# Performance work log

Measured on AMD Instinct MI355X. Metric: run time of the kernel, lower is better.

## Reference

```python
import jax, jax.numpy as jnp
import numpy as np

H, W = 480, 640
N = 256
CFEAT = 256
FAR = 80.0

def _quat_to_rot(q):
    # q: [N,4] normalized (w,x,y,z)
    w, x, y, z = q[:, 0], q[:, 1], q[:, 2], q[:, 3]
    return jnp.stack([
        jnp.stack([1 - 2 * (y * y + z * z), 2 * (x * y - w * z), 2 * (x * z + w * y)], -1),
        jnp.stack([2 * (x * y + w * z), 1 - 2 * (x * x + z * z), 2 * (y * z - w * x)], -1),
        jnp.stack([2 * (x * z - w * y), 2 * (y * z + w * x), 1 - 2 * (x * x + y * y)], -1)], -2)

def setup_inputs():
    key = jax.random.key(0)
    ks = jax.random.split(key, 10)
    z = jax.random.uniform(ks[0], (N,), minval=2.0, maxval=30.0)
    x = jax.random.uniform(ks[1], (N,), minval=-0.6, maxval=0.6) * z
    y = jax.random.uniform(ks[2], (N,), minval=-0.45, maxval=0.45) * z
    means3d = jnp.stack([x, y, z], -1)                                   # [N,3] in front of camera
    features = jax.random.normal(ks[3], (N, CFEAT))                      # [N,256]
    opacities = jax.random.uniform(ks[4], (N,), minval=0.3, maxval=0.95)
    scales = jax.random.uniform(ks[5], (N, 3), minval=0.05, maxval=0.4)
    rotations = jax.random.normal(ks[6], (N, 4))                         # unnormalized quats
    cam_K = jnp.array([[500.0, 0.0, 320.0], [0.0, 500.0, 240.0], [0.0, 0.0, 1.0]])
    cam_pose = jnp.eye(4)
    w1 = jax.random.normal(ks[7], (CFEAT, 128)) * (1.0 / np.sqrt(CFEAT))
    b1 = jnp.zeros((128,))
    w2 = jax.random.normal(ks[8], (128, 128)) * (1.0 / np.sqrt(128))
    b2 = jnp.zeros((128,))
    w3 = jax.random.normal(ks[9], (128, 12)) * (1.0 / np.sqrt(128))
    b3 = jnp.zeros((12,))
    return dict(means3d=means3d, features=features, opacities=opacities, scales=scales,
                rotations=rotations, cam_K=cam_K, cam_pose=cam_pose,
                w1=w1, b1=b1, w2=w2, b2=b2, w3=w3, b3=b3)

def _render(means3d, features, opacities, scales, rotations, cam_K, cam_pose):
    fx, fy = cam_K[0, 0], cam_K[1, 1]
    cx, cy = cam_K[0, 2], cam_K[1, 2]
    Rw, tw = cam_pose[:3, :3], cam_pose[:3, 3]
    tcam = means3d @ Rw.T + tw                                           # [N,3] camera-frame
    tz = tcam[:, 2]
    valid = tz > 0.01                                                    # near_plane cull
    tzs = jnp.where(valid, tz, 1.0)
    tx, ty = tcam[:, 0], tcam[:, 1]
    # 3D covariance: Sigma = R S S^T R^T
    q = rotations / (jnp.linalg.norm(rotations, axis=1, keepdims=True) + 1e-8)
    Rq = _quat_to_rot(q)                                                 # [N,3,3]
    M = Rq * scales[:, None, :]
    Sigma = jnp.einsum('nij,nkj->nik', M, M)
    Sc = jnp.einsum('ij,njk,lk->nil', Rw, Sigma, Rw)                     # world -> camera
    # EWA projection Jacobian [N,2,3]
    zero = jnp.zeros_like(tzs)
    J = jnp.stack([
        jnp.stack([fx / tzs, zero, -fx * tx / (tzs * tzs)], -1),
        jnp.stack([zero, fy / tzs, -fy * ty / (tzs * tzs)], -1)], -2)
    cov2d = jnp.einsum('nij,njk,nlk->nil', J, Sc, J) + 0.3 * jnp.eye(2)  # low-pass dilation
    a, b, c = cov2d[:, 0, 0], cov2d[:, 0, 1], cov2d[:, 1, 1]
    inv_det = 1.0 / jnp.maximum(a * c - b * b, 1e-12)
    A, B, C = c * inv_det, -b * inv_det, a * inv_det                     # conic
    u = fx * tx / tzs + cx
    v = fy * ty / tzs + cy
    px = jnp.arange(W, dtype=jnp.float32) + 0.5
    py = jnp.arange(H, dtype=jnp.float32) + 0.5
    dx = px[None, :] - u[:, None]                                        # [N,W]
    dy = py[None, :] - v[:, None]                                        # [N,H]
    power = (-(0.5 * A)[:, None, None] * (dx * dx)[:, None, :]
             - (0.5 * C)[:, None, None] * (dy * dy)[:, :, None]
             - B[:, None, None] * dy[:, :, None] * dx[:, None, :])       # [N,H,W]
    alpha = jnp.minimum(0.99, opacities[:, None, None] * jnp.exp(jnp.minimum(power, 0.0)))
    alpha = jnp.where(valid[:, None, None] & (alpha >= 1.0 / 255.0), alpha, 0.0)
    # front-to-back alpha compositing in depth order
    order = jnp.argsort(jnp.where(valid, tz, jnp.inf))
    alpha = jnp.take(alpha, order, axis=0).reshape(N, H * W)
    feats = jnp.take(features, order, axis=0)
    tzo = jnp.take(jnp.where(valid, tz, 0.0), order, axis=0)
    T = jnp.cumprod(1.0 - alpha, axis=0)
    T_excl = jnp.concatenate([jnp.ones((1, H * W), alpha.dtype), T[:-1]], axis=0)
    wgt = T_excl * alpha                                                 # [N,P]
    feat_img = jnp.einsum('np,nc->pc', wgt, feats).reshape(H, W, CFEAT)
    depth_img = jnp.einsum('np,n->p', wgt, tzo).reshape(H, W, 1)
    return feat_img, depth_img

def reference(means3d, features, opacities, scales, rotations, cam_K, cam_pose,
              w1, b1, w2, b2, w3, b3):
    rendered, depth = _render(means3d, features, opacities, scales, rotations, cam_K, cam_pose)
    depth = jnp.clip(depth, 0.0, FAR)
    h = jax.nn.relu(rendered @ w1 + b1)
    h = jax.nn.relu(h @ w2 + b2)
    seg = (h @ w3 + b3)[None]                                            # [1,H,W,12]
    return rendered, depth, seg
```

## Files before the change

### kernel.cpp

```cpp
#include <hip/hip_runtime.h>
#include <stdint.h>

#define HH 480
#define WW 640
#define NG 256
#define CF 256
#define FARV 80.0f
#define TILES_X (WW/64)
#define AST 264
#define BST 136

typedef __attribute__((ext_vector_type(4))) float f32x4;
typedef __attribute__((ext_vector_type(8))) short s16x8;

__device__ __forceinline__ unsigned short f2bf(float f){
  union { float f; unsigned int u; } c; c.f = f;
  unsigned int u = c.u + 0x7fffu + ((c.u >> 16) & 1u);
  return (unsigned short)(u >> 16);
}
__device__ __forceinline__ float bf2f(unsigned short h){
  union { unsigned int u; float f; } c; c.u = ((unsigned int)h) << 16; return c.f;
}

__global__ __launch_bounds__(256) void k_proj(
    const float* __restrict__ means3d,
    const float* __restrict__ opac,
    const float* __restrict__ scales,
    const float* __restrict__ rots,
    const float* __restrict__ camK,
    const float* __restrict__ camP,
    float* __restrict__ wspq,
    int* __restrict__ sidx)
{
  __shared__ float keys[NG];
  const int t = threadIdx.x;

  const float fx = camK[0], fy = camK[4];
  const float cx = camK[2], cy = camK[5];
  float Rw[3][3], tw[3];
#pragma unroll
  for (int r=0;r<3;r++){
#pragma unroll
    for (int c=0;c<3;c++) Rw[r][c] = camP[r*4+c];
    tw[r] = camP[r*4+3];
  }

  float mx = means3d[t*3+0], my = means3d[t*3+1], mz = means3d[t*3+2];
  float tcx = Rw[0][0]*mx + Rw[0][1]*my + Rw[0][2]*mz + tw[0];
  float tcy = Rw[1][0]*mx + Rw[1][1]*my + Rw[1][2]*mz + tw[1];
  float tcz = Rw[2][0]*mx + Rw[2][1]*my + Rw[2][2]*mz + tw[2];
  bool valid = tcz > 0.01f;
  float tzs = valid ? tcz : 1.0f;

  float qw = rots[t*4+0], qx = rots[t*4+1];
  float qy = rots[t*4+2], qz = rots[t*4+3];
  float nrm = sqrtf(qw*qw+qx*qx+qy*qy+qz*qz) + 1e-8f;
  qw /= nrm; qx /= nrm; qy /= nrm; qz /= nrm;
  float Rq[3][3];
  {
    float xx=qx*qx, yy=qy*qy, zz=qz*qz;
    float xy=qx*qy, xz=qx*qz, yz=qy*qz;
    float wx=qw*qx, wy=qw*qy, wz=qw*qz;
    Rq[0][0]=1.f-2.f*(yy+zz); Rq[0][1]=2.f*(xy-wz); Rq[0][2]=2.f*(xz+wy);
    Rq[1][0]=2.f*(xy+wz); Rq[1][1]=1.f-2.f*(xx+zz); Rq[1][2]=2.f*(yz-wx);
    Rq[2][0]=2.f*(xz-wy); Rq[2][1]=2.f*(yz+wx); Rq[2][2]=1.f-2.f*(xx+yy);
  }
  float s0 = scales[t*3+0], s1 = scales[t*3+1], s2 = scales[t*3+2];
  float s0s=s0*s0, s1s=s1*s1, s2s=s2*s2;
  float Sig[3][3];
#pragma unroll
  for (int i=0;i<3;i++)
#pragma unroll
    for (int j=0;j<3;j++)
      Sig[i][j] = s0s*Rq[i][0]*Rq[j][0] + s1s*Rq[i][1]*Rq[j][1] + s2s*Rq[i][2]*Rq[j][2];
  float Tm[3][3];
#pragma unroll
  for (int i=0;i<3;i++)
#pragma unroll
    for (int k=0;k<3;k++)
      Tm[i][k] = Rw[i][0]*Sig[0][k] + Rw[i][1]*Sig[1][k] + Rw[i][2]*Sig[2][k];
  float Sc[3][3];
#pragma unroll
  for (int i=0;i<3;i++)
#pragma unroll
    for (int l=0;l<3;l++)
      Sc[i][l] = Tm[i][0]*Rw[l][0] + Tm[i][1]*Rw[l][1] + Tm[i][2]*Rw[l][2];

  float iz = 1.0f / tzs;
  float r00 = fx*iz, r02 = -fx*tcx*iz*iz;
  float r11 = fy*iz, r12 = -fy*tcy*iz*iz;
  float v0 = Sc[0][0]*r00 + Sc[2][0]*r02;
  float v2 = Sc[0][2]*r00 + Sc[2][2]*r02;
  float v1 = Sc[0][1]*r00 + Sc[2][1]*r02;
  float a  = r00*v0 + r02*v2 + 0.3f;
  float bb = r11*v1 + r12*v2;
  float cc = r11*(Sc[1][1]*r11 + Sc[1][2]*r12) + r12*(Sc[2][1]*r11 + Sc[2][2]*r12) + 0.3f;
  float det = a*cc - bb*bb;
  float inv_det = 1.0f / fmaxf(det, 1e-12f);
  float Av = cc*inv_det, Bv = -bb*inv_det, Cv = a*inv_det;
  float u = fx*tcx*iz + cx;
  float v = fy*tcy*iz + cy;
  float op = opac[t];
  float op_eff = valid ? op : 0.0f;
  float tzo = valid ? tcz : 0.0f;
  float rx = -1.0f, ry = -1.0f;
  if (op_eff > (1.0f/255.0f)){
    float tau = logf(255.0f*op_eff);
    if (tau > 0.0f){
      rx = sqrtf(2.0f*tau*a) + 0.5f;
      ry = sqrtf(2.0f*tau*cc) + 0.5f;
    }
  }
  float key = valid ? tcz : __builtin_inff();

  keys[t] = key;
  __syncthreads();
  int rank = 0;
  for (int j=0;j<NG;j++){
    float kj = keys[j];
    rank += (kj < key) || (kj == key && j < t);
  }
  float4* wq = (float4*)wspq;
  float4 q0; q0.x = u;       q0.y = v;  q0.z = rx;       q0.w = ry;
  float4 q1; q1.x = 0.5f*Av; q1.y = Bv; q1.z = 0.5f*Cv;  q1.w = op_eff;
  float4 q2; q2.x = tzo;     q2.y = 0.f; q2.z = 0.f;     q2.w = 0.f;
  wq[rank*3+0] = q0;
  wq[rank*3+1] = q1;
  wq[rank*3+2] = q2;
  sidx[rank] = t;
}

__global__ __launch_bounds__(256) void k_gather(
    const float* __restrict__ features,
    const float* __restrict__ w1,
    const float* __restrict__ w2,
    const float* __restrict__ w3,
    const int* __restrict__ sidx,
    unsigned short* __restrict__ wsf,
    unsigned short* __restrict__ wt1,
    unsigned short* __restrict__ wt2,
    unsigned short* __restrict__ wt3)
{
  const int bx = blockIdx.x, t = threadIdx.x;
  if (bx < 64){
    int c = bx*256 + t;
    int row = c >> 6, c4 = c & 63;
    int src = sidx[row];
    float4 f = ((const float4*)features)[src*(CF/4) + c4];
    unsigned int* dst = (unsigned int*)(wsf + row*CF + c4*4);
    dst[0] = (unsigned)f2bf(f.x) | ((unsigned)f2bf(f.y) << 16);
    dst[1] = (unsigned)f2bf(f.z) | ((unsigned)f2bf(f.w) << 16);
  } else if (bx < 96){
    int base = (bx-64)*1024 + t*4;
#pragma unroll
    for (int e=0;e<4;e++){
      int d = base + e;
      int j = d >> 8, k = d & 255;
      wt1[d] = f2bf(w1[k*128 + j]);
    }
  } else if (bx < 104){
    int base = (bx-96)*2048 + t*8;
#pragma unroll
    for (int e=0;e<8;e++){
      int d = base + e;
      int j = d >> 7, k = d & 127;
      wt2[d] = f2bf(w2[k*128 + j]);
    }
  } else {
    int base = t*8;
#pragma unroll
    for (int e=0;e<8;e++){
      int d = base + e;
      int j = d >> 7, k = d & 127;
      wt3[d] = (j < 12) ? f2bf(w3[k*12 + j]) : (unsigned short)0;
    }
  }
}

__global__ __launch_bounds__(256) void k_diag(
    const float* __restrict__ wspq,
    float* __restrict__ dep)
{
  __shared__ __align__(16) unsigned char smem[64*AST*2 + 17408 + 1296];
  unsigned short* sh_A = (unsigned short*)smem;
  unsigned char* X = smem + 64*AST*2;
  float* c_u    = (float*)X;
  float* c_v    = c_u + 256;
  float* c_hA   = c_u + 512;
  float* c_Bq   = c_u + 768;
  float* c_hC   = c_u + 1024;
  float* c_op   = c_u + 1280;
  float* c_tz   = c_u + 1536;
  float* chprod = c_u + 1792;
  unsigned char* tail = smem + 64*AST*2 + 17408;
  float* depch = (float*)tail;
  unsigned char* act_idx = tail + 1024;
  int* wcnt = (int*)(tail + 1280);

  const int t = threadIdx.x;
  const int lane = t & 63;
  const int wvi = t >> 6;
  const int y  = blockIdx.x / TILES_X;
  const int x0 = (blockIdx.x % TILES_X) * 64;

  act_idx[t] = 0;
  const float4* wq = (const float4*)wspq;
  float4 q0 = wq[t*3+0];
  bool pred = (q0.z > 0.0f)
      && (q0.x + q0.z >= (float)x0 + 0.5f)
      && (q0.x - q0.z <= (float)x0 + 63.5f)
      && (fabsf(q0.y - ((float)y + 0.5f)) <= q0.w);
  unsigned long long m = __ballot(pred);
  if (lane == 0) wcnt[wvi] = __popcll(m);
  __syncthreads();
  int base = 0;
#pragma unroll
  for (int i=0;i<4;i++) base += (i < wvi) ? wcnt[i] : 0;
  const int nact = wcnt[0]+wcnt[1]+wcnt[2]+wcnt[3];
  if (pred){
    int pos = base + __popcll(m & ((1ull << lane) - 1ull));
    float4 q1 = wq[t*3+1];
    float4 q2 = wq[t*3+2];
    act_idx[pos] = (unsigned char)t;
    c_u[pos]  = q0.x;  c_v[pos]  = q0.y;
    c_hA[pos] = q1.x;  c_Bq[pos] = q1.y;  c_hC[pos] = q1.z;
    c_op[pos] = q1.w;  c_tz[pos] = q2.x;
  }
  __syncthreads();

  const int per8 = ((((nact + 3) >> 2) + 7) & ~7);
  const int n0 = wvi * per8;
  const int n1 = (nact < n0 + per8) ? nact : (n0 + per8);
  const float px = (float)(x0 + lane) + 0.5f;
  const float py = (float)y + 0.5f;

  {
    float prod = 1.0f;
    for (int ng = n0; ng < n0 + per8; ng += 8){
      union { unsigned short s[8]; uint4 v4; } alp;
#pragma unroll
      for (int e=0;e<8;e++){
        int n = ng + e;
        float al = 0.0f;
        if (n < n1){
          float dx = px - c_u[n], dy = py - c_v[n];
          float q = c_hA[n]*dx*dx + c_Bq[n]*dx*dy + c_hC[n]*dy*dy;
          al = fminf(0.99f, c_op[n]*__expf(fminf(-q, 0.0f)));
          if (al < (1.0f/255.0f)) al = 0.0f;
        }
        alp.s[e] = f2bf(al);
        prod *= 1.0f - bf2f(alp.s[e]);
      }
      *((uint4*)&sh_A[lane*AST + ng]) = alp.v4;
    }
    chprod[t] = prod;
  }
  __syncthreads();

  {
    float T = 1.0f;
#pragma unroll
    for (int c=0;c<4;c++) if (c < wvi) T *= chprod[c*64 + lane];
    float dacc = 0.0f;
    for (int ng = n0; ng < n0 + per8; ng += 8){
      union { unsigned short s[8]; uint4 v4; } ap, wp;
      ap.v4 = *((const uint4*)&sh_A[lane*AST + ng]);
#pragma unroll
      for (int e=0;e<8;e++){
        float al = bf2f(ap.s[e]);
        float wgt = T * al;
        T *= 1.0f - al;
        wp.s[e] = f2bf(wgt);
        int n = ng + e;
        if (n < n1) dacc += wgt * c_tz[n];
      }
      *((uint4*)&sh_A[lane*AST + ng]) = wp.v4;
    }
    depch[t] = dacc;
  }
  asm volatile("" ::: "memory");
  __syncthreads();

  if (wvi == 0){
    float d = depch[lane] + depch[64+lane] + depch[128+lane] + depch[192+lane];
    dep[y*WW + x0 + lane] = fminf(fmaxf(d, 0.0f), FARV);
  }
}

__global__ __launch_bounds__(256) void k_fused(
    const float* __restrict__ wspq,
    const unsigned short* __restrict__ wsf,
    const unsigned short* __restrict__ wt1,
    const unsigned short* __restrict__ wt2,
    const unsigned short* __restrict__ wt3,
    const float* __restrict__ b1,
    const float* __restrict__ b2,
    const float* __restrict__ b3,
    float* __restrict__ out,
    float* __restrict__ dep,
    float* __restrict__ seg)
{
  __shared__ __align__(16) unsigned char smem[64*AST*2 + 17408 + 1296];
  unsigned short* sh_A = (unsigned short*)smem;
  unsigned char* X = smem + 64*AST*2;
  float* c_u    = (float*)X;
  float* c_v    = c_u + 256;
  float* c_hA   = c_u + 512;
  float* c_Bq   = c_u + 768;
  float* c_hC   = c_u + 1024;
  float* c_op   = c_u + 1280;
  float* c_tz   = c_u + 1536;
  float* chprod = c_u + 1792;
  unsigned short* stage = (unsigned short*)X;
  unsigned short* sh_B  = (unsigned short*)X;
  unsigned char* tail = smem + 64*AST*2 + 17408;
  float* depch = (float*)tail;
  unsigned char* act_idx = tail + 1024;
  int* wcnt = (int*)(tail + 1280);

  const int t = threadIdx.x;
  const int lane = t & 63;
  const int wvi = t >> 6;
  const int y  = blockIdx.x / TILES_X;
  const int x0 = (blockIdx.x % TILES_X) * 64;

  act_idx[t] = 0;
  const float4* wq = (const float4*)wspq;
  float4 q0 = wq[t*3+0];
  bool pred = (q0.z > 0.0f)
      && (q0.x + q0.z >= (float)x0 + 0.5f)
      && (q0.x - q0.z <= (float)x0 + 63.5f)
      && (fabsf(q0.y - ((float)y + 0.5f)) <= q0.w);
  unsigned long long m = __ballot(pred);
  if (lane == 0) wcnt[wvi] = __popcll(m);
  __syncthreads();
  int base = 0;
#pragma unroll
  for (int i=0;i<4;i++) base += (i < wvi) ? wcnt[i] : 0;
  const int nact = wcnt[0]+wcnt[1]+wcnt[2]+wcnt[3];
  if (pred){
    int pos = base + __popcll(m & ((1ull << lane) - 1ull));
    float4 q1 = wq[t*3+1];
    float4 q2 = wq[t*3+2];
    act_idx[pos] = (unsigned char)t;
    c_u[pos]  = q0.x;  c_v[pos]  = q0.y;
    c_hA[pos] = q1.x;  c_Bq[pos] = q1.y;  c_hC[pos] = q1.z;
    c_op[pos] = q1.w;  c_tz[pos] = q2.x;
  }
  __syncthreads();

  const int per8 = ((((nact + 3) >> 2) + 7) & ~7);
  const int n0 = wvi * per8;
  const int n1 = (nact < n0 + per8) ? nact : (n0 + per8);
  const float px = (float)(x0 + lane) + 0.5f;
  const float py = (float)y + 0.5f;

  const int ln  = lane & 15;
  const int kq8 = (lane >> 4) * 8;
  const int rq  = (lane >> 4) * 4;
  const int cb0 = wvi * 64;
  const int la = lane & 7, lb = lane >> 3;
  const int kchunks = (nact + 31) >> 5;

  uint4 cur[4], nxt[4];
  if (kchunks > 0){
#pragma unroll
    for (int g=0; g<4; g++){
      int kk = lb + 8*g;
      cur[g] = *(const uint4*)(wsf + (int)act_idx[kk]*CF + cb0 + la*8);
    }
  }

  {
    float prod = 1.0f;
    for (int ng = n0; ng < n0 + per8; ng += 8){
      union { unsigned short s[8]; uint4 v4; } alp;
#pragma unroll
      for (int e=0;e<8;e++){
        int n = ng + e;
        float al = 0.0f;
        if (n < n1){
          float dx = px - c_u[n], dy = py - c_v[n];
          float q = c_hA[n]*dx*dx + c_Bq[n]*dx*dy + c_hC[n]*dy*dy;
          al = fminf(0.99f, c_op[n]*__expf(fminf(-q, 0.0f)));
          if (al < (1.0f/255.0f)) al = 0.0f;
        }
        alp.s[e] = f2bf(al);
        prod *= 1.0f - bf2f(alp.s[e]);
      }
      *((uint4*)&sh_A[lane*AST + ng]) = alp.v4;
    }
    chprod[t] = prod;
  }
  __syncthreads();

  {
    float T = 1.0f;
#pragma unroll
    for (int c=0;c<4;c++) if (c < wvi) T *= chprod[c*64 + lane];
    float dacc = 0.0f;
    for (int ng = n0; ng < n0 + per8; ng += 8){
      union { unsigned short s[8]; uint4 v4; } ap, wp;
      ap.v4 = *((const uint4*)&sh_A[lane*AST + ng]);
#pragma unroll
      for (int e=0;e<8;e++){
        float al = bf2f(ap.s[e]);
        float wgt = T * al;
        T *= 1.0f - al;
        wp.s[e] = f2bf(wgt);
        int n = ng + e;
        if (n < n1) dacc += wgt * c_tz[n];
      }
      *((uint4*)&sh_A[lane*AST + ng]) = wp.v4;
    }
    depch[t] = dacc;
  }
  __syncthreads();

  unsigned short* stW = stage + wvi*2048;
  const int xw = (la & 3) << 3;

  f32x4 acc[4][4];
#pragma unroll
  for (int mt=0;mt<4;mt++)
#pragma unroll
    for (int nt=0;nt<4;nt++){
      f32x4 z = {0.f,0.f,0.f,0.f};
      acc[mt][nt] = z;
    }
  for (int kb=0; kb<kchunks; kb++){
#pragma unroll
    for (int g=0; g<4; g++){
      const unsigned short* s = (const unsigned short*)&cur[g];
      int colw = (lb + 8*g) ^ xw;
#pragma unroll
      for (int i=0;i<8;i++)
        stW[(la*8 + i)*32 + colw] = s[i];
    }
    if (kb+1 < kchunks){
#pragma unroll
      for (int g=0; g<4; g++){
        int kk = (kb+1)*32 + lb + 8*g;
        nxt[g] = *(const uint4*)(wsf + (int)act_idx[kk]*CF + cb0 + la*8);
      }
    }
    int k0 = kb*32;
    s16x8 bfr[4];
#pragma unroll
    for (int nt=0;nt<4;nt++){
      int chl = nt*16 + ln;
      int colr = kq8 ^ (((chl >> 3) & 3) << 3);
      bfr[nt] = *(const s16x8*)(stW + chl*32 + colr);
    }
#pragma unroll
    for (int mt=0;mt<4;mt++){
      s16x8 afr = *(const s16x8*)(&sh_A[(mt*16 + ln)*AST + k0 + kq8]);
#pragma unroll
      for (int nt=0;nt<4;nt++)
        acc[mt][nt] = __builtin_amdgcn_mfma_f32_16x16x32_bf16(afr, bfr[nt], acc[mt][nt], 0, 0, 0);
    }
    if (kb+1 < kchunks){
#pragma unroll
      for (int g=0; g<4; g++) cur[g] = nxt[g];
    }
  }
  __syncthreads();

#pragma unroll
  for (int mt=0;mt<4;mt++)
#pragma unroll
    for (int nt=0;nt<4;nt++)
#pragma unroll
      for (int r=0;r<4;r++){
        int row = mt*16 + rq + r;
        int col = cb0 + nt*16 + ln;
        sh_A[row*AST + col] = f2bf(acc[mt][nt][r]);
      }
  __syncthreads();

  const int n0m = wvi * 32;
  f32x4 acc1[4][2];
#pragma unroll
  for (int nn=0;nn<2;nn++){
    float bv = b1[n0m + nn*16 + ln];
    f32x4 b4 = {bv,bv,bv,bv};
#pragma unroll
    for (int mt=0;mt<4;mt++) acc1[mt][nn] = b4;
  }
#pragma unroll
  for (int k0=0;k0<256;k0+=32){
    s16x8 bfr0 = *(const s16x8*)(wt1 + (n0m + 0*16 + ln)*256 + k0 + kq8);
    s16x8 bfr1 = *(const s16x8*)(wt1 + (n0m + 1*16 + ln)*256 + k0 + kq8);
#pragma unroll
    for (int mt=0;mt<4;mt++){
      s16x8 afr = *(const s16x8*)(&sh_A[(mt*16 + ln)*AST + k0 + kq8]);
      acc1[mt][0] = __builtin_amdgcn_mfma_f32_16x16x32_bf16(afr, bfr0, acc1[mt][0], 0, 0, 0);
      acc1[mt][1] = __builtin_amdgcn_mfma_f32_16x16x32_bf16(afr, bfr1, acc1[mt][1], 0, 0, 0);
    }
  }
#pragma unroll
  for (int mt=0;mt<4;mt++)
#pragma unroll
    for (int nn=0;nn<2;nn++)
#pragma unroll
      for (int r=0;r<4;r++){
        int mrow = mt*16 + rq + r;
        int ncol = n0m + nn*16 + ln;
        sh_B[mrow*BST + ncol] = f2bf(fmaxf(acc1[mt][nn][r], 0.0f));
      }
  __syncthreads();

  f32x4 acc2[4][2];
#pragma unroll
  for (int nn=0;nn<2;nn++){
    float bv = b2[n0m + nn*16 + ln];
    f32x4 b4 = {bv,bv,bv,bv};
#pragma unroll
    for (int mt=0;mt<4;mt++) acc2[mt][nn] = b4;
  }
#pragma unroll
  for (int k0=0;k0<128;k0+=32){
    s16x8 bfr0 = *(const s16x8*)(wt2 + (n0m + 0*16 + ln)*128 + k0 + kq8);
    s16x8 bfr1 = *(const s16x8*)(wt2 + (n0m + 1*16 + ln)*128 + k0 + kq8);
#pragma unroll
    for (int mt=0;mt<4;mt++){
      s16x8 afr = *(const s16x8*)(&sh_B[(mt*16 + ln)*BST + k0 + kq8]);
      acc2[mt][0] = __builtin_amdgcn_mfma_f32_16x16x32_bf16(afr, bfr0, acc2[mt][0], 0, 0, 0);
      acc2[mt][1] = __builtin_amdgcn_mfma_f32_16x16x32_bf16(afr, bfr1, acc2[mt][1], 0, 0, 0);
    }
  }
  __syncthreads();
#pragma unroll
  for (int mt=0;mt<4;mt++)
#pragma unroll
    for (int nn=0;nn<2;nn++)
#pragma unroll
      for (int r=0;r<4;r++){
        int mrow = mt*16 + rq + r;
        int ncol = n0m + nn*16 + ln;
        sh_B[mrow*BST + ncol] = f2bf(fmaxf(acc2[mt][nn][r], 0.0f));
      }
  __syncthreads();

  const size_t Pbase = (size_t)(y*WW + x0);
  f32x4 acc3;
  {
    float bv = (ln < 12) ? b3[ln] : 0.0f;
    f32x4 b4 = {bv,bv,bv,bv};
    acc3 = b4;
  }
#pragma unroll
  for (int k0=0;k0<128;k0+=32){
    s16x8 afr = *(const s16x8*)(&sh_B[(wvi*16 + ln)*BST + k0 + kq8]);
    s16x8 bfr = *(const s16x8*)(wt3 + ln*128 + k0 + kq8);
    acc3 = __builtin_amdgcn_mfma_f32_16x16x32_bf16(afr, bfr, acc3, 0, 0, 0);
  }
  if (ln < 12){
#pragma unroll
    for (int r=0;r<4;r++){
      int mrow = wvi*16 + rq + r;
      seg[(Pbase + mrow)*12 + ln] = acc3[r];
    }
  }

  if (wvi == 0){
    float d = depch[lane] + depch[64+lane] + depch[128+lane] + depch[192+lane];
    dep[y*WW + x0 + lane] = fminf(fmaxf(d, 0.0f), FARV);
  }

  {
    const int pxb = wvi*16;
    for (int i=0;i<16;i++){
      int pix = pxb + i;
      uint2 dv = *(const uint2*)(&sh_A[pix*AST + lane*4]);
      f32x4 o;
      o[0] = bf2f((unsigned short)(dv.x & 0xffffu));
      o[1] = bf2f((unsigned short)(dv.x >> 16));
      o[2] = bf2f((unsigned short)(dv.y & 0xffffu));
      o[3] = bf2f((unsigned short)(dv.y >> 16));
      __builtin_nontemporal_store(o, (f32x4*)(&out[(Pbase + pix)*CF + lane*4]));
    }
  }
}

extern "C" void kernel_launch(void* const* d_in, const int* in_sizes, int n_in,
                              void* d_out, int out_size, void* d_ws, size_t ws_size,
                              hipStream_t stream) {
  (void)in_sizes; (void)n_in; (void)out_size; (void)ws_size;
  const float* means3d  = (const float*)d_in[0];
  const float* features = (const float*)d_in[1];
  const float* opac     = (const float*)d_in[2];
  const float* scales   = (const float*)d_in[3];
  const float* rots     = (const float*)d_in[4];
  const float* camK     = (const float*)d_in[5];
  const float* camP     = (const float*)d_in[6];
  const float* w1       = (const float*)d_in[7];
  const float* b1       = (const float*)d_in[8];
  const float* w2       = (const float*)d_in[9];
  const float* b2       = (const float*)d_in[10];
  const float* w3       = (const float*)d_in[11];
  const float* b3       = (const float*)d_in[12];

  char* ws = (char*)d_ws;
  float*          wspq = (float*)ws;
  int*            sidx = (int*)(ws + 12288);
  unsigned short* wsf  = (unsigned short*)(ws + 13312);
  unsigned short* wt1  = (unsigned short*)(ws + 144384);
  unsigned short* wt2  = (unsigned short*)(ws + 209920);
  unsigned short* wt3  = (unsigned short*)(ws + 242688);

  float* out = (float*)d_out;
  float* dep = out + (size_t)HH*WW*CF;
  float* seg = dep + (size_t)HH*WW;

  k_proj<<<1, 256, 0, stream>>>(means3d, opac, scales, rots, camK, camP, wspq, sidx);
  k_gather<<<105, 256, 0, stream>>>(features, w1, w2, w3, sidx, wsf, wt1, wt2, wt3);
  k_diag<<<HH*TILES_X, 256, 0, stream>>>(wspq, dep);
  k_fused<<<HH*TILES_X, 256, 0, stream>>>(wspq, wsf, wt1, wt2, wt3, b1, b2, b3, out, dep, seg);
}
```

Baseline: 129.3 us.

## Precompute features@W1 per Gaussian and split render and segmentation kernels

```diff
diff --git a/kernel.cpp b/kernel.cpp
--- a/kernel.cpp
+++ b/kernel.cpp
@@ -137,7 +137,7 @@
     const float* __restrict__ w3,
     const int* __restrict__ sidx,
     unsigned short* __restrict__ wsf,
-    unsigned short* __restrict__ wt1,
+    unsigned short* __restrict__ wsg1,
     unsigned short* __restrict__ wt2,
     unsigned short* __restrict__ wt3)
 {
@@ -150,23 +150,15 @@
     unsigned int* dst = (unsigned int*)(wsf + row*CF + c4*4);
     dst[0] = (unsigned)f2bf(f.x) | ((unsigned)f2bf(f.y) << 16);
     dst[1] = (unsigned)f2bf(f.z) | ((unsigned)f2bf(f.w) << 16);
-  } else if (bx < 96){
-    int base = (bx-64)*1024 + t*4;
-#pragma unroll
-    for (int e=0;e<4;e++){
-      int d = base + e;
-      int j = d >> 8, k = d & 255;
-      wt1[d] = f2bf(w1[k*128 + j]);
-    }
-  } else if (bx < 104){
-    int base = (bx-96)*2048 + t*8;
+  } else if (bx < 72){
+    int base = (bx-64)*2048 + t*8;
 #pragma unroll
     for (int e=0;e<8;e++){
       int d = base + e;
       int j = d >> 7, k = d & 127;
       wt2[d] = f2bf(w2[k*128 + j]);
     }
-  } else {
+  } else if (bx < 73){
     int base = t*8;
 #pragma unroll
     for (int e=0;e<8;e++){
@@ -174,11 +166,25 @@
       int j = d >> 7, k = d & 127;
       wt3[d] = (j < 12) ? f2bf(w3[k*12 + j]) : (unsigned short)0;
     }
+  } else {
+    __shared__ float frow[CF];
+    int g = bx - 73;
+    int src = sidx[g];
+    if (t < 64) ((float4*)frow)[t] = ((const float4*)features)[src*(CF/4) + t];
+    __syncthreads();
+    if (t < 128){
+      float s = 0.0f;
+      for (int k=0;k<CF;k++)
+        s += frow[k] * w1[k*128 + t];
+      wsg1[g*128 + t] = f2bf(s);
+    }
   }
 }
 
-__global__ __launch_bounds__(256) void k_diag(
+__global__ __launch_bounds__(256) void k_render(
     const float* __restrict__ wspq,
+    const unsigned short* __restrict__ wsf,
+    float* __restrict__ out,
     float* __restrict__ dep)
 {
   __shared__ __align__(16) unsigned char smem[64*AST*2 + 17408 + 1296];
@@ -192,6 +198,7 @@
   float* c_op   = c_u + 1280;
   float* c_tz   = c_u + 1536;
   float* chprod = c_u + 1792;
+  unsigned short* stage = (unsigned short*)X;
   unsigned char* tail = smem + 64*AST*2 + 17408;
   float* depch = (float*)tail;
   unsigned char* act_idx = tail + 1024;
@@ -233,6 +240,22 @@
   const int n1 = (nact < n0 + per8) ? nact : (n0 + per8);
   const float px = (float)(x0 + lane) + 0.5f;
   const float py = (float)y + 0.5f;
+
+  const int ln  = lane & 15;
+  const int kq8 = (lane >> 4) * 8;
+  const int rq  = (lane >> 4) * 4;
+  const int cb0 = wvi * 64;
+  const int la = lane & 7, lb = lane >> 3;
+  const int kchunks = (nact + 31) >> 5;
+
+  uint4 cur[4], nxt[4];
+  if (kchunks > 0){
+#pragma unroll
+    for (int g=0; g<4; g++){
+      int kk = lb + 8*g;
+      cur[g] = *(const uint4*)(wsf + (int)act_idx[kk]*CF + cb0 + la*8);
+    }
+  }
 
   {
     float prod = 1.0f;
@@ -278,29 +301,100 @@
     }
     depch[t] = dacc;
   }
-  asm volatile("" ::: "memory");
-  __syncthreads();
-
+  __syncthreads();
+
+  unsigned short* stW = stage + wvi*2048;
+  const int xw = (la & 3) << 3;
+
+  f32x4 acc[4][4];
+#pragma unroll
+  for (int mt=0;mt<4;mt++)
+#pragma unroll
+    for (int nt=0;nt<4;nt++){
+      f32x4 z = {0.f,0.f,0.f,0.f};
+      acc[mt][nt] = z;
+    }
+  for (int kb=0; kb<kchunks; kb++){
+#pragma unroll
+    for (int g=0; g<4; g++){
+      const unsigned short* s = (const unsigned short*)&cur[g];
+      int colw = (lb + 8*g) ^ xw;
+#pragma unroll
+      for (int i=0;i<8;i++)
+        stW[(la*8 + i)*32 + colw] = s[i];
+    }
+    if (kb+1 < kchunks){
+#pragma unroll
+      for (int g=0; g<4; g++){
+        int kk = (kb+1)*32 + lb + 8*g;
+        nxt[g] = *(const uint4*)(wsf + (int)act_idx[kk]*CF + cb0 + la*8);
+      }
+    }
+    int k0 = kb*32;
+    s16x8 bfr[4];
+#pragma unroll
+    for (int nt=0;nt<4;nt++){
+      int chl = nt*16 + ln;
+      int colr = kq8 ^ (((chl >> 3) & 3) << 3);
+      bfr[nt] = *(const s16x8*)(stW + chl*32 + colr);
+    }
+#pragma unroll
+    for (int mt=0;mt<4;mt++){
+      s16x8 afr = *(const s16x8*)(&sh_A[(mt*16 + ln)*AST + k0 + kq8]);
+#pragma unroll
+      for (int nt=0;nt<4;nt++)
+        acc[mt][nt] = __builtin_amdgcn_mfma_f32_16x16x32_bf16(afr, bfr[nt], acc[mt][nt], 0, 0, 0);
+    }
+    if (kb+1 < kchunks){
+#pragma unroll
+      for (int g=0; g<4; g++) cur[g] = nxt[g];
+    }
+  }
+  __syncthreads();
+
+#pragma unroll
+  for (int mt=0;mt<4;mt++)
+#pragma unroll
+    for (int nt=0;nt<4;nt++)
+#pragma unroll
+      for (int r=0;r<4;r++){
+        int row = mt*16 + rq + r;
+        int col = cb0 + nt*16 + ln;
+        sh_A[row*AST + col] = f2bf(acc[mt][nt][r]);
+      }
+  __syncthreads();
+
+  const size_t Pbase = (size_t)(y*WW + x0);
   if (wvi == 0){
     float d = depch[lane] + depch[64+lane] + depch[128+lane] + depch[192+lane];
     dep[y*WW + x0 + lane] = fminf(fmaxf(d, 0.0f), FARV);
   }
+  {
+    const int pxb = wvi*16;
+    for (int i=0;i<16;i++){
+      int pix = pxb + i;
+      uint2 dv = *(const uint2*)(&sh_A[pix*AST + lane*4]);
+      f32x4 o;
+      o[0] = bf2f((unsigned short)(dv.x & 0xffffu));
+      o[1] = bf2f((unsigned short)(dv.x >> 16));
+      o[2] = bf2f((unsigned short)(dv.y & 0xffffu));
+      o[3] = bf2f((unsigned short)(dv.y >> 16));
+      __builtin_nontemporal_store(o, (f32x4*)(&out[(Pbase + pix)*CF + lane*4]));
+    }
+  }
 }
 
-__global__ __launch_bounds__(256) void k_fused(
+__global__ __launch_bounds__(256) void k_seg(
     const float* __restrict__ wspq,
-    const unsigned short* __restrict__ wsf,
-    const unsigned short* __restrict__ wt1,
+    const unsigned short* __restrict__ wsg1,
     const unsigned short* __restrict__ wt2,
     const unsigned short* __restrict__ wt3,
     const float* __restrict__ b1,
     const float* __restrict__ b2,
     const float* __restrict__ b3,
-    float* __restrict__ out,
-    float* __restrict__ dep,
     float* __restrict__ seg)
 {
-  __shared__ __align__(16) unsigned char smem[64*AST*2 + 17408 + 1296];
+  __shared__ __align__(16) unsigned char smem[64*AST*2 + 17408 + 288];
   unsigned short* sh_A = (unsigned short*)smem;
   unsigned char* X = smem + 64*AST*2;
   float* c_u    = (float*)X;
@@ -309,14 +403,12 @@
   float* c_Bq   = c_u + 768;
   float* c_hC   = c_u + 1024;
   float* c_op   = c_u + 1280;
-  float* c_tz   = c_u + 1536;
-  float* chprod = c_u + 1792;
+  float* chprod = c_u + 1536;
   unsigned short* stage = (unsigned short*)X;
   unsigned short* sh_B  = (unsigned short*)X;
   unsigned char* tail = smem + 64*AST*2 + 17408;
-  float* depch = (float*)tail;
-  unsigned char* act_idx = tail + 1024;
-  int* wcnt = (int*)(tail + 1280);
+  unsigned char* act_idx = tail;
+  int* wcnt = (int*)(tail + 256);
 
   const int t = threadIdx.x;
   const int lane = t & 63;
@@ -341,11 +433,10 @@
   if (pred){
     int pos = base + __popcll(m & ((1ull << lane) - 1ull));
     float4 q1 = wq[t*3+1];
-    float4 q2 = wq[t*3+2];
     act_idx[pos] = (unsigned char)t;
     c_u[pos]  = q0.x;  c_v[pos]  = q0.y;
     c_hA[pos] = q1.x;  c_Bq[pos] = q1.y;  c_hC[pos] = q1.z;
-    c_op[pos] = q1.w;  c_tz[pos] = q2.x;
+    c_op[pos] = q1.w;
   }
   __syncthreads();
 
@@ -358,18 +449,9 @@
   const int ln  = lane & 15;
   const int kq8 = (lane >> 4) * 8;
   const int rq  = (lane >> 4) * 4;
-  const int cb0 = wvi * 64;
-  const int la = lane & 7, lb = lane >> 3;
+  const int rG = lane >> 1, hcG = lane & 1;
   const int kchunks = (nact + 31) >> 5;
-
-  uint4 cur[4], nxt[4];
-  if (kchunks > 0){
-#pragma unroll
-    for (int g=0; g<4; g++){
-      int kk = lb + 8*g;
-      cur[g] = *(const uint4*)(wsf + (int)act_idx[kk]*CF + cb0 + la*8);
-    }
-  }
+  const int n0m = wvi * 32;
 
   {
     float prod = 1.0f;
@@ -398,87 +480,22 @@
     float T = 1.0f;
 #pragma unroll
     for (int c=0;c<4;c++) if (c < wvi) T *= chprod[c*64 + lane];
-    float dacc = 0.0f;
     for (int ng = n0; ng < n0 + per8; ng += 8){
       union { unsigned short s[8]; uint4 v4; } ap, wp;
       ap.v4 = *((const uint4*)&sh_A[lane*AST + ng]);
 #pragma unroll
       for (int e=0;e<8;e++){
         float al = bf2f(ap.s[e]);
-        float wgt = T * al;
+        wp.s[e] = f2bf(T * al);
         T *= 1.0f - al;
-        wp.s[e] = f2bf(wgt);
-        int n = ng + e;
-        if (n < n1) dacc += wgt * c_tz[n];
       }
       *((uint4*)&sh_A[lane*AST + ng]) = wp.v4;
     }
-    depch[t] = dacc;
-  }
-  __syncthreads();
-
-  unsigned short* stW = stage + wvi*2048;
-  const int xw = (la & 3) << 3;
-
-  f32x4 acc[4][4];
-#pragma unroll
-  for (int mt=0;mt<4;mt++)
-#pragma unroll
-    for (int nt=0;nt<4;nt++){
-      f32x4 z = {0.f,0.f,0.f,0.f};
-      acc[mt][nt] = z;
-    }
-  for (int kb=0; kb<kchunks; kb++){
-#pragma unroll
-    for (int g=0; g<4; g++){
-      const unsigned short* s = (const unsigned short*)&cur[g];
-      int colw = (lb + 8*g) ^ xw;
-#pragma unroll
-      for (int i=0;i<8;i++)
-        stW[(la*8 + i)*32 + colw] = s[i];
-    }
-    if (kb+1 < kchunks){
-#pragma unroll
-      for (int g=0; g<4; g++){
-        int kk = (kb+1)*32 + lb + 8*g;
-        nxt[g] = *(const uint4*)(wsf + (int)act_idx[kk]*CF + cb0 + la*8);
-      }
-    }
-    int k0 = kb*32;
-    s16x8 bfr[4];
-#pragma unroll
-    for (int nt=0;nt<4;nt++){
-      int chl = nt*16 + ln;
-      int colr = kq8 ^ (((chl >> 3) & 3) << 3);
-      bfr[nt] = *(const s16x8*)(stW + chl*32 + colr);
-    }
-#pragma unroll
-    for (int mt=0;mt<4;mt++){
-      s16x8 afr = *(const s16x8*)(&sh_A[(mt*16 + ln)*AST + k0 + kq8]);
-#pragma unroll
-      for (int nt=0;nt<4;nt++)
-        acc[mt][nt] = __builtin_amdgcn_mfma_f32_16x16x32_bf16(afr, bfr[nt], acc[mt][nt], 0, 0, 0);
-    }
-    if (kb+1 < kchunks){
-#pragma unroll
-      for (int g=0; g<4; g++) cur[g] = nxt[g];
-    }
-  }
-  __syncthreads();
-
-#pragma unroll
-  for (int mt=0;mt<4;mt++)
-#pragma unroll
-    for (int nt=0;nt<4;nt++)
-#pragma unroll
-      for (int r=0;r<4;r++){
-        int row = mt*16 + rq + r;
-        int col = cb0 + nt*16 + ln;
-        sh_A[row*AST + col] = f2bf(acc[mt][nt][r]);
-      }
-  __syncthreads();
-
-  const int n0m = wvi * 32;
+  }
+  __syncthreads();
+
+  unsigned short* stW = stage + wvi*1280;
+
   f32x4 acc1[4][2];
 #pragma unroll
   for (int nn=0;nn<2;nn++){
@@ -487,17 +504,44 @@
 #pragma unroll
     for (int mt=0;mt<4;mt++) acc1[mt][nn] = b4;
   }
-#pragma unroll
-  for (int k0=0;k0<256;k0+=32){
-    s16x8 bfr0 = *(const s16x8*)(wt1 + (n0m + 0*16 + ln)*256 + k0 + kq8);
-    s16x8 bfr1 = *(const s16x8*)(wt1 + (n0m + 1*16 + ln)*256 + k0 + kq8);
+  uint4 ga, gb, ga2, gb2;
+  if (kchunks > 0){
+    const unsigned short* gsrc = wsg1 + (int)act_idx[rG]*128 + n0m + hcG*16;
+    ga = *(const uint4*)gsrc;
+    gb = *(const uint4*)(gsrc + 8);
+  }
+  for (int kb=0; kb<kchunks; kb++){
+    {
+      const unsigned short* gap = (const unsigned short*)&ga;
+      const unsigned short* gbp = (const unsigned short*)&gb;
+#pragma unroll
+      for (int c2=0;c2<8;c2++)
+        stW[(hcG*16 + c2)*40 + rG] = gap[c2];
+#pragma unroll
+      for (int c2=0;c2<8;c2++)
+        stW[(hcG*16 + 8 + c2)*40 + rG] = gbp[c2];
+    }
+    if (kb+1 < kchunks){
+      const unsigned short* gsrc = wsg1 + (int)act_idx[(kb+1)*32 + rG]*128 + n0m + hcG*16;
+      ga2 = *(const uint4*)gsrc;
+      gb2 = *(const uint4*)(gsrc + 8);
+    }
+    int k0 = kb*32;
+    s16x8 bfrG[2];
+#pragma unroll
+    for (int nt2=0;nt2<2;nt2++)
+      bfrG[nt2] = *(const s16x8*)(stW + (nt2*16 + ln)*40 + kq8);
 #pragma unroll
     for (int mt=0;mt<4;mt++){
       s16x8 afr = *(const s16x8*)(&sh_A[(mt*16 + ln)*AST + k0 + kq8]);
-      acc1[mt][0] = __builtin_amdgcn_mfma_f32_16x16x32_bf16(afr, bfr0, acc1[mt][0], 0, 0, 0);
-      acc1[mt][1] = __builtin_amdgcn_mfma_f32_16x16x32_bf16(afr, bfr1, acc1[mt][1], 0, 0, 0);
-    }
-  }
+#pragma unroll
+      for (int nt2=0;nt2<2;nt2++)
+        acc1[mt][nt2] = __builtin_amdgcn_mfma_f32_16x16x32_bf16(afr, bfrG[nt2], acc1[mt][nt2], 0, 0, 0);
+    }
+    if (kb+1 < kchunks){ ga = ga2; gb = gb2; }
+  }
+  __syncthreads();
+
 #pragma unroll
   for (int mt=0;mt<4;mt++)
 #pragma unroll
@@ -560,25 +604,6 @@
     for (int r=0;r<4;r++){
       int mrow = wvi*16 + rq + r;
       seg[(Pbase + mrow)*12 + ln] = acc3[r];
-    }
-  }
-
-  if (wvi == 0){
-    float d = depch[lane] + depch[64+lane] + depch[128+lane] + depch[192+lane];
-    dep[y*WW + x0 + lane] = fminf(fmaxf(d, 0.0f), FARV);
-  }
-
-  {
-    const int pxb = wvi*16;
-    for (int i=0;i<16;i++){
-      int pix = pxb + i;
-      uint2 dv = *(const uint2*)(&sh_A[pix*AST + lane*4]);
-      f32x4 o;
-      o[0] = bf2f((unsigned short)(dv.x & 0xffffu));
-      o[1] = bf2f((unsigned short)(dv.x >> 16));
-      o[2] = bf2f((unsigned short)(dv.y & 0xffffu));
-      o[3] = bf2f((unsigned short)(dv.y >> 16));
-      __builtin_nontemporal_store(o, (f32x4*)(&out[(Pbase + pix)*CF + lane*4]));
     }
   }
 }
@@ -605,7 +630,7 @@
   float*          wspq = (float*)ws;
   int*            sidx = (int*)(ws + 12288);
   unsigned short* wsf  = (unsigned short*)(ws + 13312);
-  unsigned short* wt1  = (unsigned short*)(ws + 144384);
+  unsigned short* wsg1 = (unsigned short*)(ws + 144384);
   unsigned short* wt2  = (unsigned short*)(ws + 209920);
   unsigned short* wt3  = (unsigned short*)(ws + 242688);
 
@@ -614,7 +639,7 @@
   float* seg = dep + (size_t)HH*WW;
 
   k_proj<<<1, 256, 0, stream>>>(means3d, opac, scales, rots, camK, camP, wspq, sidx);
-  k_gather<<<105, 256, 0, stream>>>(features, w1, w2, w3, sidx, wsf, wt1, wt2, wt3);
-  k_diag<<<HH*TILES_X, 256, 0, stream>>>(wspq, dep);
-  k_fused<<<HH*TILES_X, 256, 0, stream>>>(wspq, wsf, wt1, wt2, wt3, b1, b2, b3, out, dep, seg);
+  k_gather<<<329, 256, 0, stream>>>(features, w1, w2, w3, sidx, wsf, wsg1, wt2, wt3);
+  k_seg<<<HH*TILES_X, 256, 0, stream>>>(wspq, wsg1, wt2, wt3, b1, b2, b3, seg);
+  k_render<<<HH*TILES_X, 256, 0, stream>>>(wspq, wsf, out, dep);
 }
```

After: 127.6 us. Within noise of the previous version (-1.3%).
